# Kernel tuning notes

Hardware: AMD Instinct MI355X
Metric: run time of the kernel (lower is better)

## Reference

```python
import jax, jax.numpy as jnp
import numpy as np
from jax import lax

PATCH = 17
THRESH = 0.5


def _bbox_from_mask(mask_np):
    # mask_np: [D,H,W] bool. Matches mask_to_3d_bbox (min/max of nonzero coords).
    z, y, x = np.nonzero(mask_np)
    return (int(x.min()), int(y.min()), int(z.min()),
            int(x.max()), int(y.max()), int(z.max()))


def _extract_patches(vol, bbox):
    # vol: [1,1,D,H,W]; crop uses exclusive max (slice z_min:z_max) like the torch code
    x0, y0, z0, x1, y1, z1 = bbox
    t = vol[:, :, z0:z1, y0:y1, x0:x1]
    pads = []
    for d in t.shape[2:]:
        r = d % PATCH
        p = (PATCH - r) % PATCH
        pads.append((p // 2, p - p // 2))
    t = jnp.pad(t, ((0, 0), (0, 0), pads[0], pads[1], pads[2]))
    D, H, W = t.shape[2:]
    nD, nH, nW = D // PATCH, H // PATCH, W // PATCH
    p = t.reshape(nD, PATCH, nH, PATCH, nW, PATCH)
    p = p.transpose(0, 2, 4, 1, 3, 5).reshape(-1, PATCH, PATCH, PATCH)
    return p[:, None]  # [N,1,17,17,17]


def _conv3d(x, w, b, stride):
    y = lax.conv_general_dilated(x, w, (stride,) * 3, 'VALID',
                                 dimension_numbers=('NCDHW', 'OIDHW', 'NCDHW'))
    return y + b.reshape(1, -1, 1, 1, 1)


def _model(fixed, moving, c1w, c1b, c2w, c2b, f1w, f1b, f2w, f2b):
    # Stand-in for the opaque torch.jit model: siamese-concat 3D CNN -> MLP -> tanh.
    x = jnp.concatenate([fixed, moving], axis=1)          # [N,2,17,17,17]
    x = jax.nn.relu(_conv3d(x, c1w, c1b, 2))              # [N,32,8,8,8]
    x = jax.nn.relu(_conv3d(x, c2w, c2b, 2))              # [N,64,3,3,3]
    x = x.reshape(x.shape[0], -1)                         # [N,1728]
    x = jax.nn.relu(x @ f1w.T + f1b)                      # [N,256]
    return jnp.tanh(x @ f2w.T + f2b)                      # [N,1]


def setup_inputs() -> dict:
    key = jax.random.key(0)
    ks = jax.random.split(key, 10)
    V = 222
    source = jax.random.normal(ks[0], (1, 1, V, V, V), jnp.float32)
    target = jax.random.uniform(ks[1], (1, 1, V, V, V), jnp.float32)
    fc_in = 64 * 3 * 3 * 3
    return {
        'source': source,
        'target': target,
        'conv1_w': jax.random.normal(ks[2], (32, 2, 3, 3, 3), jnp.float32) * 0.1,
        'conv1_b': jnp.zeros((32,), jnp.float32),
        'conv2_w': jax.random.normal(ks[3], (64, 32, 3, 3, 3), jnp.float32) * 0.05,
        'conv2_b': jnp.zeros((64,), jnp.float32),
        'fc1_w': jax.random.normal(ks[4], (256, fc_in), jnp.float32) * 0.02,
        'fc1_b': jnp.zeros((256,), jnp.float32),
        'fc2_w': jax.random.normal(ks[5], (1, 256), jnp.float32) * 0.05,
        'fc2_b': jnp.zeros((1,), jnp.float32),
    }


def reference(source, target, conv1_w, conv1_b, conv2_w, conv2_b,
              fc1_w, fc1_b, fc2_w, fc2_b):
    mask_np = np.asarray(target) > 0
    bbox = _bbox_from_mask(mask_np.squeeze())
    fixed_patches = _extract_patches(target, bbox)   # [N,1,17,17,17]
    moving_patches = _extract_patches(source, bbox)
    # per-patch zero fraction on fixed patches; keep if <= threshold
    zero_frac = jnp.mean((fixed_patches[:, 0] == 0).astype(jnp.float32), axis=(1, 2, 3))
    keep = (zero_frac <= THRESH).astype(jnp.float32)  # [N]
    out = _model(fixed_patches, moving_patches, conv1_w, conv1_b, conv2_w, conv2_b,
                 fc1_w, fc1_b, fc2_w, fc2_b)          # [N,1]
    # mean over kept patches == weighted mean (stream-compaction-free, same math)
    return jnp.sum(out[:, 0] * keep) / jnp.sum(keep)
```

## Files before the change

kernel.cpp:

```cpp
#include <hip/hip_runtime.h>


static constexpr int kPS = 433;
static constexpr int kRS = 25;
static constexpr int kCS = 528;
static constexpr int kZS = 66;

__global__ __launch_bounds__(256, 4)
void DMMRLoss_52621939310662_kernel(
    const float* __restrict__ src, const float* __restrict__ tgt,
    const float* __restrict__ c1w, const float* __restrict__ c1b,
    const float* __restrict__ c2w, const float* __restrict__ c2b,
    float* __restrict__ h2, float* __restrict__ pk) {
  __shared__ float sBuf[8704];
  __shared__ float sRed[256];
  int p = blockIdx.x;
  int t = threadIdx.x;
  int pd = p / 169; int rem = p - pd * 169; int phh = rem / 13; int pww = rem - phh * 13;
  int z0 = pd * 17, y0 = phh * 17, x0 = pww * 17;

  int wv  = t >> 6;
  int od  = (t >> 3) & 7, oh = t & 7;
  int oc2 = t & 63;

  float cnt = 0.f;
  for (int idx = t; idx < 4913; idx += 256) {
    int a = idx / 289; int r2 = idx - a * 289; int b = r2 / 17; int c = r2 - b * 17;
    float v = tgt[((size_t)(z0 + a) * 222 + (y0 + b)) * 222 + (x0 + c)];
    sBuf[a * kPS + b * kRS + c] = v;
    if (v == 0.0f) cnt += 1.f;
  }
  sRed[t] = cnt;
  __syncthreads();
  for (int o = 128; o > 0; o >>= 1) {
    if (t < o) sRed[t] += sRed[t + o];
    __syncthreads();
  }
  float keep = (sRed[0] / 4913.0f <= 0.5f) ? 1.0f : 0.0f;
  if (t == 0) pk[p] = keep;
  __syncthreads();

  float acc2[27];
  #pragma unroll
  for (int i = 0; i < 27; i++) acc2[i] = 0.f;

  #pragma unroll 1
  for (int half = 0; half < 2; half++) {
    float acc[4][8];
    #pragma unroll
    for (int i = 0; i < 4; i++)
      #pragma unroll
      for (int j = 0; j < 8; j++) acc[i][j] = 0.f;

    #pragma unroll 1
    for (int ic = 0; ic < 2; ic++) {
      if (half + ic > 0) {
        const float* vol = ic ? src : tgt;
        __syncthreads();
        for (int idx = t; idx < 4913; idx += 256) {
          int a = idx / 289; int r2 = idx - a * 289; int b = r2 / 17; int c = r2 - b * 17;
          sBuf[a * kPS + b * kRS + c] =
              vol[((size_t)(z0 + a) * 222 + (y0 + b)) * 222 + (x0 + c)];
        }
        __syncthreads();
      }
      #pragma unroll 1
      for (int td = 0; td < 3; td++) {
        #pragma unroll 1
        for (int th = 0; th < 3; th++) {
          int rbase = (2 * od + td) * kPS + (2 * oh + th) * kRS;
          float a[17];
          #pragma unroll
          for (int x = 0; x < 17; x++) a[x] = sBuf[rbase + x];
          #pragma unroll
          for (int ocr = 0; ocr < 4; ocr++) {
            int oc = half * 16 + wv * 4 + ocr;
            const float* wp = c1w + oc * 54 + ic * 27 + td * 9 + th * 3;
            float w0 = wp[0], w1 = wp[1], w2 = wp[2];
            #pragma unroll
            for (int ow = 0; ow < 8; ow++)
              acc[ocr][ow] += a[2 * ow] * w0 + a[2 * ow + 1] * w1 + a[2 * ow + 2] * w2;
          }
        }
      }
    }
    __syncthreads();
    #pragma unroll
    for (int ocr = 0; ocr < 4; ocr++) {
      int lo = wv * 4 + ocr;
      float b = c1b[half * 16 + lo];
      int base = lo * kCS + od * kZS + oh * 8;
      #pragma unroll
      for (int ow = 0; ow < 8; ow++)
        sBuf[base + ow] = fmaxf(acc[ocr][ow] + b, 0.f);
    }
    __syncthreads();

    #pragma unroll 1
    for (int icr = 0; icr < 4; icr++) {
      int icl = wv * 4 + icr;
      int ic  = half * 16 + icl;
      const float* cbase = sBuf + icl * kCS;
      #pragma unroll 1
      for (int td = 0; td < 3; td++) {
        #pragma unroll 1
        for (int th = 0; th < 3; th++) {
          const float* wp = c2w + oc2 * 864 + ic * 27 + td * 9 + th * 3;
          float w0 = wp[0], w1 = wp[1], w2 = wp[2];
          #pragma unroll
          for (int zo = 0; zo < 3; zo++) {
            #pragma unroll
            for (int yo = 0; yo < 3; yo++) {
              const float* rp = cbase + (2 * zo + td) * kZS + (2 * yo + th) * 8;
              #pragma unroll
              for (int xo = 0; xo < 3; xo++)
                acc2[zo * 9 + yo * 3 + xo] +=
                    rp[2 * xo] * w0 + rp[2 * xo + 1] * w1 + rp[2 * xo + 2] * w2;
            }
          }
        }
      }
    }
  }
  __syncthreads();
  #pragma unroll
  for (int pos = 0; pos < 27; pos++)
    sBuf[(wv * 27 + pos) * 64 + oc2] = acc2[pos];
  __syncthreads();
  float* h2p = h2 + (size_t)p * 1728;
  for (int idx = t; idx < 1728; idx += 256) {
    int o = idx & 63, pos = idx >> 6;
    float v = sBuf[pos * 64 + o] + sBuf[(27 + pos) * 64 + o] +
              sBuf[(54 + pos) * 64 + o] + sBuf[(81 + pos) * 64 + o];
    h2p[idx] = fmaxf(v + c2b[o], 0.f);
  }
}

__global__ void dmr22_pack(const float* __restrict__ f1w, float* __restrict__ wp4) {
  int k4 = blockIdx.x;
  int n  = threadIdx.x;
  float4 w;
  float* pw = (float*)&w;
  #pragma unroll
  for (int j = 0; j < 4; j++) {
    int kp = k4 * 4 + j;
    int o = kp & 63, pos = kp >> 6;
    pw[j] = f1w[(size_t)n * 1728 + (o * 27 + pos)];
  }
  ((float4*)wp4)[(size_t)k4 * 256 + n] = w;
}

static constexpr int kKT = 192;
static constexpr int kTS = 36;

__global__ __launch_bounds__(256, 4)
void dmr22_gemm(const float* __restrict__ h2, const float* __restrict__ wp4,
                const float* __restrict__ f1b, const float* __restrict__ f2w,
                float* __restrict__ part) {
  __shared__ float sT[kKT * kTS];
  int b = blockIdx.x;
  int pg = b >> 2, ng = b & 3;
  int p0 = pg * 32;
  int t = threadIdx.x;
  int n = ng * 64 + (t & 63);
  int pgrp = t >> 6;

  float acc[8];
  #pragma unroll
  for (int i = 0; i < 8; i++) acc[i] = 0.f;

  #pragma unroll 1
  for (int kt = 0; kt < 1728; kt += kKT) {
    __syncthreads();
    #pragma unroll 1
    for (int i = 0; i < (32 * kKT) / 256; i++) {
      int idx = i * 256 + t;
      int pp = idx / kKT, kk = idx - pp * kKT;
      sT[kk * kTS + pp] = h2[(size_t)(p0 + pp) * 1728 + kt + kk];
    }
    __syncthreads();
    #pragma unroll 2
    for (int k4 = 0; k4 < kKT / 4; k4++) {
      float4 w = ((const float4*)wp4)[(size_t)((kt >> 2) + k4) * 256 + n];
      const float* r0 = sT + (k4 * 4 + 0) * kTS + pgrp * 8;
      const float* r1 = sT + (k4 * 4 + 1) * kTS + pgrp * 8;
      const float* r2 = sT + (k4 * 4 + 2) * kTS + pgrp * 8;
      const float* r3 = sT + (k4 * 4 + 3) * kTS + pgrp * 8;
      float4 a0 = *(const float4*)r0, b0 = *(const float4*)(r0 + 4);
      float4 a1 = *(const float4*)r1, b1 = *(const float4*)(r1 + 4);
      float4 a2 = *(const float4*)r2, b2 = *(const float4*)(r2 + 4);
      float4 a3 = *(const float4*)r3, b3 = *(const float4*)(r3 + 4);
      acc[0] += w.x * a0.x + w.y * a1.x + w.z * a2.x + w.w * a3.x;
      acc[1] += w.x * a0.y + w.y * a1.y + w.z * a2.y + w.w * a3.y;
      acc[2] += w.x * a0.z + w.y * a1.z + w.z * a2.z + w.w * a3.z;
      acc[3] += w.x * a0.w + w.y * a1.w + w.z * a2.w + w.w * a3.w;
      acc[4] += w.x * b0.x + w.y * b1.x + w.z * b2.x + w.w * b3.x;
      acc[5] += w.x * b0.y + w.y * b1.y + w.z * b2.y + w.w * b3.y;
      acc[6] += w.x * b0.z + w.y * b1.z + w.z * b2.z + w.w * b3.z;
      acc[7] += w.x * b0.w + w.y * b1.w + w.z * b2.w + w.w * b3.w;
    }
  }
  float b1v = f1b[n], w2v = f2w[n];
  #pragma unroll
  for (int pp = 0; pp < 8; pp++) {
    float tl = fmaxf(acc[pp] + b1v, 0.f) * w2v;
    #pragma unroll
    for (int o = 32; o > 0; o >>= 1) tl += __shfl_down(tl, o, 64);
    if ((t & 63) == 0)
      part[(size_t)(p0 + pgrp * 8 + pp) * 4 + ng] = tl;
  }
}

__global__ void dmr22_fin(const float* __restrict__ part, const float* __restrict__ pk,
                          const float* __restrict__ f2b, float* __restrict__ out) {
  __shared__ float s1[256], s2[256];
  int t = threadIdx.x;
  float b0 = f2b[0];
  float a = 0.f, b = 0.f;
  for (int p = t; p < 2197; p += 256) {
    float s = part[4 * p] + part[4 * p + 1] + part[4 * p + 2] + part[4 * p + 3];
    float kv = pk[p];
    a += tanhf(s + b0) * kv;
    b += kv;
  }
  s1[t] = a; s2[t] = b;
  __syncthreads();
  for (int o = 128; o > 0; o >>= 1) {
    if (t < o) { s1[t] += s1[t + o]; s2[t] += s2[t + o]; }
    __syncthreads();
  }
  if (t == 0) out[0] = s1[0] / s2[0];
}

__global__ __launch_bounds__(256, 2)
void dmr22_solo(const float* __restrict__ src, const float* __restrict__ tgt,
                const float* __restrict__ c1w, const float* __restrict__ c1b,
                const float* __restrict__ c2w, const float* __restrict__ c2b,
                const float* __restrict__ f1w, const float* __restrict__ f1b,
                const float* __restrict__ f2w, const float* __restrict__ f2b,
                float* __restrict__ out) {
  __shared__ float sBuf[8704];
  __shared__ float sH[1728];
  __shared__ float sRed[256];
  __shared__ float sAcc[2];
  int t = threadIdx.x;
  int wv = t >> 6, od = (t >> 3) & 7, oh = t & 7, oc2 = t & 63;
  if (t == 0) { sAcc[0] = 0.f; sAcc[1] = 0.f; }
  for (int p = 0; p < 2197; p++) {
    __syncthreads();
    int pd = p / 169; int rem = p - pd * 169; int phh = rem / 13; int pww = rem - phh * 13;
    int z0 = pd * 17, y0 = phh * 17, x0 = pww * 17;
    float cnt = 0.f;
    for (int idx = t; idx < 4913; idx += 256) {
      int a = idx / 289; int r2 = idx - a * 289; int b = r2 / 17; int c = r2 - b * 17;
      float v = tgt[((size_t)(z0 + a) * 222 + (y0 + b)) * 222 + (x0 + c)];
      sBuf[a * kPS + b * kRS + c] = v;
      if (v == 0.0f) cnt += 1.f;
    }
    sRed[t] = cnt;
    __syncthreads();
    for (int o = 128; o > 0; o >>= 1) {
      if (t < o) sRed[t] += sRed[t + o];
      __syncthreads();
    }
    float keep = (sRed[0] / 4913.0f <= 0.5f) ? 1.0f : 0.0f;
    __syncthreads();
    float acc2[27];
    for (int i = 0; i < 27; i++) acc2[i] = 0.f;
    #pragma unroll 1
    for (int half = 0; half < 2; half++) {
      float acc[4][8];
      for (int i = 0; i < 4; i++)
        for (int j = 0; j < 8; j++) acc[i][j] = 0.f;
      #pragma unroll 1
      for (int ic = 0; ic < 2; ic++) {
        if (half + ic > 0) {
          const float* vol = ic ? src : tgt;
          __syncthreads();
          for (int idx = t; idx < 4913; idx += 256) {
            int a = idx / 289; int r2 = idx - a * 289; int b = r2 / 17; int c = r2 - b * 17;
            sBuf[a * kPS + b * kRS + c] =
                vol[((size_t)(z0 + a) * 222 + (y0 + b)) * 222 + (x0 + c)];
          }
          __syncthreads();
        }
        #pragma unroll 1
        for (int td = 0; td < 3; td++) {
          #pragma unroll 1
          for (int th = 0; th < 3; th++) {
            int rbase = (2 * od + td) * kPS + (2 * oh + th) * kRS;
            float a[17];
            #pragma unroll
            for (int x = 0; x < 17; x++) a[x] = sBuf[rbase + x];
            #pragma unroll
            for (int ocr = 0; ocr < 4; ocr++) {
              int oc = half * 16 + wv * 4 + ocr;
              const float* wp = c1w + oc * 54 + ic * 27 + td * 9 + th * 3;
              float w0 = wp[0], w1 = wp[1], w2 = wp[2];
              #pragma unroll
              for (int ow = 0; ow < 8; ow++)
                acc[ocr][ow] += a[2 * ow] * w0 + a[2 * ow + 1] * w1 + a[2 * ow + 2] * w2;
            }
          }
        }
      }
      __syncthreads();
      #pragma unroll
      for (int ocr = 0; ocr < 4; ocr++) {
        int lo = wv * 4 + ocr;
        float b = c1b[half * 16 + lo];
        int base = lo * kCS + od * kZS + oh * 8;
        #pragma unroll
        for (int ow = 0; ow < 8; ow++)
          sBuf[base + ow] = fmaxf(acc[ocr][ow] + b, 0.f);
      }
      __syncthreads();
      #pragma unroll 1
      for (int icr = 0; icr < 4; icr++) {
        int icl = wv * 4 + icr;
        int ic  = half * 16 + icl;
        const float* cbase = sBuf + icl * kCS;
        #pragma unroll 1
        for (int td = 0; td < 3; td++) {
          #pragma unroll 1
          for (int th = 0; th < 3; th++) {
            const float* wp = c2w + oc2 * 864 + ic * 27 + td * 9 + th * 3;
            float w0 = wp[0], w1 = wp[1], w2 = wp[2];
            #pragma unroll
            for (int zo = 0; zo < 3; zo++) {
              #pragma unroll
              for (int yo = 0; yo < 3; yo++) {
                const float* rp = cbase + (2 * zo + td) * kZS + (2 * yo + th) * 8;
                #pragma unroll
                for (int xo = 0; xo < 3; xo++)
                  acc2[zo * 9 + yo * 3 + xo] +=
                      rp[2 * xo] * w0 + rp[2 * xo + 1] * w1 + rp[2 * xo + 2] * w2;
              }
            }
          }
        }
      }
    }
    __syncthreads();
    #pragma unroll
    for (int pos = 0; pos < 27; pos++)
      sBuf[(wv * 27 + pos) * 64 + oc2] = acc2[pos];
    __syncthreads();
    for (int idx = t; idx < 1728; idx += 256) {
      int o = idx & 63, pos = idx >> 6;
      float v = sBuf[pos * 64 + o] + sBuf[(27 + pos) * 64 + o] +
                sBuf[(54 + pos) * 64 + o] + sBuf[(81 + pos) * 64 + o];
      sH[o * 27 + pos] = fmaxf(v + c2b[o], 0.f);
    }
    __syncthreads();
    float acc1 = 0.f;
    const float* frow = f1w + (size_t)t * 1728;
    #pragma unroll 8
    for (int k = 0; k < 1728; k++) acc1 += sH[k] * frow[k];
    float h = fmaxf(acc1 + f1b[t], 0.f);
    sRed[t] = h * f2w[t];
    __syncthreads();
    for (int o = 128; o > 0; o >>= 1) {
      if (t < o) sRed[t] += sRed[t + o];
      __syncthreads();
    }
    if (t == 0) {
      sAcc[0] += tanhf(sRed[0] + f2b[0]) * keep;
      sAcc[1] += keep;
    }
  }
  __syncthreads();
  if (t == 0) out[0] = sAcc[0] / sAcc[1];
}

extern "C" void kernel_launch(void* const* d_in, const int* in_sizes, int n_in,
                              void* d_out, int out_size, void* d_ws, size_t ws_size,
                              hipStream_t stream) {
  const float* src = (const float*)d_in[0];
  const float* tgt = (const float*)d_in[1];
  const float* c1w = (const float*)d_in[2];
  const float* c1b = (const float*)d_in[3];
  const float* c2w = (const float*)d_in[4];
  const float* c2b = (const float*)d_in[5];
  const float* f1w = (const float*)d_in[6];
  const float* f1b = (const float*)d_in[7];
  const float* f2w = (const float*)d_in[8];
  const float* f2b = (const float*)d_in[9];
  float* out = (float*)d_out;

  const size_t nWP  = 442368;
  const size_t nH2  = (size_t)2208 * 1728;
  const size_t nPart = 2208 * 4;
  const size_t nPk  = 2208;
  if (d_ws && ws_size >= (nWP + nH2 + nPart + nPk) * sizeof(float)) {
    float* wp4  = (float*)d_ws;
    float* h2   = wp4 + nWP;
    float* part = h2 + nH2;
    float* pk   = part + nPart;
    dmr22_pack<<<432, 256, 0, stream>>>(f1w, wp4);
    DMMRLoss_52621939310662_kernel<<<2197, 256, 0, stream>>>(
        src, tgt, c1w, c1b, c2w, c2b, h2, pk);
    dmr22_gemm<<<276, 256, 0, stream>>>(h2, wp4, f1b, f2w, part);
    dmr22_fin<<<1, 256, 0, stream>>>(part, pk, f2b, out);
  } else {
    dmr22_solo<<<1, 256, 0, stream>>>(
        src, tgt, c1w, c1b, c2w, c2b, f1w, f1b, f2w, f2b, out);
  }
}
```

Measured before the change: 441.0 us.

## Restructure FC1 GEMM to row-major h2 tiles and replace tree reduction with shuffles

The FC1 GEMM now copies h2 tiles into shared memory row-major with float4 loads and no transpose. Each thread handles 4 output neurons for 2 patches, and the packed weights are reorganised as [k][n/4] float4 so each thread reads four weight vectors per k-step. The conv kernel's zero-count reduction now uses wavefront shuffles plus a 4-entry shared array, which drops the 8-step shared-memory tree and one barrier. The aim is to cut uncoalesced scalar stores and barriers during h2 staging. The cost is more weight loads per FLOP in the inner loop.

Result: faster. 420.2 us (-4.7%).

```diff
diff --git a/kernel.cpp b/kernel.cpp
--- a/kernel.cpp
+++ b/kernel.cpp
@@ -13,7 +13,7 @@
     const float* __restrict__ c2w, const float* __restrict__ c2b,
     float* __restrict__ h2, float* __restrict__ pk) {
   __shared__ float sBuf[8704];
-  __shared__ float sRed[256];
+  __shared__ float sRed[4];
   int p = blockIdx.x;
   int t = threadIdx.x;
   int pd = p / 169; int rem = p - pd * 169; int phh = rem / 13; int pww = rem - phh * 13;
@@ -30,15 +30,12 @@
     sBuf[a * kPS + b * kRS + c] = v;
     if (v == 0.0f) cnt += 1.f;
   }
-  sRed[t] = cnt;
+  #pragma unroll
+  for (int o = 32; o > 0; o >>= 1) cnt += __shfl_down(cnt, o, 64);
+  if ((t & 63) == 0) sRed[wv] = cnt;
   __syncthreads();
-  for (int o = 128; o > 0; o >>= 1) {
-    if (t < o) sRed[t] += sRed[t + o];
-    __syncthreads();
-  }
-  float keep = (sRed[0] / 4913.0f <= 0.5f) ? 1.0f : 0.0f;
+  float keep = ((sRed[0] + sRed[1] + sRed[2] + sRed[3]) / 4913.0f <= 0.5f) ? 1.0f : 0.0f;
   if (t == 0) pk[p] = keep;
-  __syncthreads();
 
   float acc2[27];
   #pragma unroll
@@ -136,82 +133,86 @@
   }
 }
 
-__global__ void dmr22_pack(const float* __restrict__ f1w, float* __restrict__ wp4) {
-  int k4 = blockIdx.x;
-  int n  = threadIdx.x;
+__global__ void dmr23_pack(const float* __restrict__ f1w, float* __restrict__ wp4) {
+  int gid = blockIdx.x * 256 + threadIdx.x;
+  int kp = gid >> 6, n4 = gid & 63;
+  int o = kp & 63, pos = kp >> 6;
+  int korig = o * 27 + pos;
   float4 w;
-  float* pw = (float*)&w;
-  #pragma unroll
-  for (int j = 0; j < 4; j++) {
-    int kp = k4 * 4 + j;
-    int o = kp & 63, pos = kp >> 6;
-    pw[j] = f1w[(size_t)n * 1728 + (o * 27 + pos)];
-  }
-  ((float4*)wp4)[(size_t)k4 * 256 + n] = w;
+  w.x = f1w[(size_t)(n4 * 4 + 0) * 1728 + korig];
+  w.y = f1w[(size_t)(n4 * 4 + 1) * 1728 + korig];
+  w.z = f1w[(size_t)(n4 * 4 + 2) * 1728 + korig];
+  w.w = f1w[(size_t)(n4 * 4 + 3) * 1728 + korig];
+  ((float4*)wp4)[gid] = w;
 }
 
 static constexpr int kKT = 192;
-static constexpr int kTS = 36;
+static constexpr int kTS = 196;
 
 __global__ __launch_bounds__(256, 4)
-void dmr22_gemm(const float* __restrict__ h2, const float* __restrict__ wp4,
+void dmr23_gemm(const float* __restrict__ h2, const float* __restrict__ wp4,
                 const float* __restrict__ f1b, const float* __restrict__ f2w,
                 float* __restrict__ part) {
-  __shared__ float sT[kKT * kTS];
+  __shared__ float sT[32 * kTS];
   int b = blockIdx.x;
   int pg = b >> 2, ng = b & 3;
   int p0 = pg * 32;
   int t = threadIdx.x;
-  int n = ng * 64 + (t & 63);
-  int pgrp = t >> 6;
-
-  float acc[8];
+  int n4l = t & 15;
+  int n4 = ng * 16 + n4l;
+  int pgrp = t >> 4;
+  int pA = pgrp * 2, pB = pA + 1;
+
+  float acc[4][2];
   #pragma unroll
-  for (int i = 0; i < 8; i++) acc[i] = 0.f;
+  for (int j = 0; j < 4; j++) { acc[j][0] = 0.f; acc[j][1] = 0.f; }
 
   #pragma unroll 1
   for (int kt = 0; kt < 1728; kt += kKT) {
     __syncthreads();
-    #pragma unroll 1
-    for (int i = 0; i < (32 * kKT) / 256; i++) {
+    #pragma unroll
+    for (int i = 0; i < 6; i++) {
       int idx = i * 256 + t;
-      int pp = idx / kKT, kk = idx - pp * kKT;
-      sT[kk * kTS + pp] = h2[(size_t)(p0 + pp) * 1728 + kt + kk];
+      int pp = idx / 48, kq = idx - pp * 48;
+      float4 v = *(const float4*)(h2 + (size_t)(p0 + pp) * 1728 + kt + kq * 4);
+      *(float4*)(sT + pp * kTS + kq * 4) = v;
     }
     __syncthreads();
     #pragma unroll 2
     for (int k4 = 0; k4 < kKT / 4; k4++) {
-      float4 w = ((const float4*)wp4)[(size_t)((kt >> 2) + k4) * 256 + n];
-      const float* r0 = sT + (k4 * 4 + 0) * kTS + pgrp * 8;
-      const float* r1 = sT + (k4 * 4 + 1) * kTS + pgrp * 8;
-      const float* r2 = sT + (k4 * 4 + 2) * kTS + pgrp * 8;
-      const float* r3 = sT + (k4 * 4 + 3) * kTS + pgrp * 8;
-      float4 a0 = *(const float4*)r0, b0 = *(const float4*)(r0 + 4);
-      float4 a1 = *(const float4*)r1, b1 = *(const float4*)(r1 + 4);
-      float4 a2 = *(const float4*)r2, b2 = *(const float4*)(r2 + 4);
-      float4 a3 = *(const float4*)r3, b3 = *(const float4*)(r3 + 4);
-      acc[0] += w.x * a0.x + w.y * a1.x + w.z * a2.x + w.w * a3.x;
-      acc[1] += w.x * a0.y + w.y * a1.y + w.z * a2.y + w.w * a3.y;
-      acc[2] += w.x * a0.z + w.y * a1.z + w.z * a2.z + w.w * a3.z;
-      acc[3] += w.x * a0.w + w.y * a1.w + w.z * a2.w + w.w * a3.w;
-      acc[4] += w.x * b0.x + w.y * b1.x + w.z * b2.x + w.w * b3.x;
-      acc[5] += w.x * b0.y + w.y * b1.y + w.z * b2.y + w.w * b3.y;
-      acc[6] += w.x * b0.z + w.y * b1.z + w.z * b2.z + w.w * b3.z;
-      acc[7] += w.x * b0.w + w.y * b1.w + w.z * b2.w + w.w * b3.w;
-    }
-  }
-  float b1v = f1b[n], w2v = f2w[n];
+      int kb = kt + k4 * 4;
+      float4 w0 = ((const float4*)wp4)[(size_t)(kb + 0) * 64 + n4];
+      float4 w1 = ((const float4*)wp4)[(size_t)(kb + 1) * 64 + n4];
+      float4 w2 = ((const float4*)wp4)[(size_t)(kb + 2) * 64 + n4];
+      float4 w3 = ((const float4*)wp4)[(size_t)(kb + 3) * 64 + n4];
+      float4 hA = *(const float4*)(sT + pA * kTS + k4 * 4);
+      float4 hB = *(const float4*)(sT + pB * kTS + k4 * 4);
+      acc[0][0] += w0.x * hA.x + w1.x * hA.y + w2.x * hA.z + w3.x * hA.w;
+      acc[1][0] += w0.y * hA.x + w1.y * hA.y + w2.y * hA.z + w3.y * hA.w;
+      acc[2][0] += w0.z * hA.x + w1.z * hA.y + w2.z * hA.z + w3.z * hA.w;
+      acc[3][0] += w0.w * hA.x + w1.w * hA.y + w2.w * hA.z + w3.w * hA.w;
+      acc[0][1] += w0.x * hB.x + w1.x * hB.y + w2.x * hB.z + w3.x * hB.w;
+      acc[1][1] += w0.y * hB.x + w1.y * hB.y + w2.y * hB.z + w3.y * hB.w;
+      acc[2][1] += w0.z * hB.x + w1.z * hB.y + w2.z * hB.z + w3.z * hB.w;
+      acc[3][1] += w0.w * hB.x + w1.w * hB.y + w2.w * hB.z + w3.w * hB.w;
+    }
+  }
+  float b0 = f1b[n4 * 4 + 0], b1 = f1b[n4 * 4 + 1];
+  float b2 = f1b[n4 * 4 + 2], b3 = f1b[n4 * 4 + 3];
+  float v0 = f2w[n4 * 4 + 0], v1 = f2w[n4 * 4 + 1];
+  float v2 = f2w[n4 * 4 + 2], v3 = f2w[n4 * 4 + 3];
   #pragma unroll
-  for (int pp = 0; pp < 8; pp++) {
-    float tl = fmaxf(acc[pp] + b1v, 0.f) * w2v;
+  for (int pp = 0; pp < 2; pp++) {
+    float tl = fmaxf(acc[0][pp] + b0, 0.f) * v0 + fmaxf(acc[1][pp] + b1, 0.f) * v1 +
+               fmaxf(acc[2][pp] + b2, 0.f) * v2 + fmaxf(acc[3][pp] + b3, 0.f) * v3;
     #pragma unroll
-    for (int o = 32; o > 0; o >>= 1) tl += __shfl_down(tl, o, 64);
-    if ((t & 63) == 0)
-      part[(size_t)(p0 + pgrp * 8 + pp) * 4 + ng] = tl;
-  }
-}
-
-__global__ void dmr22_fin(const float* __restrict__ part, const float* __restrict__ pk,
+    for (int o = 8; o > 0; o >>= 1) tl += __shfl_down(tl, o, 16);
+    if (n4l == 0)
+      part[(size_t)(p0 + pA + pp) * 4 + ng] = tl;
+  }
+}
+
+__global__ void dmr23_fin(const float* __restrict__ part, const float* __restrict__ pk,
                           const float* __restrict__ f2b, float* __restrict__ out) {
   __shared__ float s1[256], s2[256];
   int t = threadIdx.x;
@@ -233,7 +234,7 @@
 }
 
 __global__ __launch_bounds__(256, 2)
-void dmr22_solo(const float* __restrict__ src, const float* __restrict__ tgt,
+void dmr23_solo(const float* __restrict__ src, const float* __restrict__ tgt,
                 const float* __restrict__ c1w, const float* __restrict__ c1b,
                 const float* __restrict__ c2w, const float* __restrict__ c2b,
                 const float* __restrict__ f1w, const float* __restrict__ f1b,
@@ -388,22 +389,22 @@
   const float* f2b = (const float*)d_in[9];
   float* out = (float*)d_out;
 
-  const size_t nWP  = 442368;
-  const size_t nH2  = (size_t)2208 * 1728;
+  const size_t nWP   = 442368;
+  const size_t nH2   = (size_t)2208 * 1728;
   const size_t nPart = 2208 * 4;
-  const size_t nPk  = 2208;
+  const size_t nPk   = 2208;
   if (d_ws && ws_size >= (nWP + nH2 + nPart + nPk) * sizeof(float)) {
     float* wp4  = (float*)d_ws;
     float* h2   = wp4 + nWP;
     float* part = h2 + nH2;
     float* pk   = part + nPart;
-    dmr22_pack<<<432, 256, 0, stream>>>(f1w, wp4);
+    dmr23_pack<<<432, 256, 0, stream>>>(f1w, wp4);
     DMMRLoss_52621939310662_kernel<<<2197, 256, 0, stream>>>(
         src, tgt, c1w, c1b, c2w, c2b, h2, pk);
-    dmr22_gemm<<<276, 256, 0, stream>>>(h2, wp4, f1b, f2w, part);
-    dmr22_fin<<<1, 256, 0, stream>>>(part, pk, f2b, out);
+    dmr23_gemm<<<276, 256, 0, stream>>>(h2, wp4, f1b, f2w, part);
+    dmr23_fin<<<1, 256, 0, stream>>>(part, pk, f2b, out);
   } else {
-    dmr22_solo<<<1, 256, 0, stream>>>(
+    dmr23_solo<<<1, 256, 0, stream>>>(
         src, tgt, c1w, c1b, c2w, c2b, f1w, f1b, f2w, f2b, out);
   }
 }
```
